# Performance work log

Measured on AMD Instinct MI355X. Metric: run time of the kernel, lower is better.

The kernel has to match this reference:

```python
import jax, jax.numpy as jnp
import numpy as np

N_NODES = 50000
N_EDGES = 800000
IN_DIM = 256
HID = 128
OUT = 128
LEAKY_SLOPE = 0.01


def setup_inputs() -> dict:
    key = jax.random.key(0)
    ks = jax.random.split(key, 12)
    s = 0.05
    return {
        "h": jax.random.normal(ks[0], (N_NODES, IN_DIM), dtype=jnp.float32),
        "src": jax.random.randint(ks[1], (N_EDGES,), 0, N_NODES, dtype=jnp.int32),
        "dst": jax.random.randint(ks[2], (N_EDGES,), 0, N_NODES, dtype=jnp.int32),
        "W1": jax.random.normal(ks[3], (HID, IN_DIM), dtype=jnp.float32) * s,
        "b1": jax.random.normal(ks[4], (HID,), dtype=jnp.float32) * s,
        "a1": jax.random.normal(ks[5], (2 * HID,), dtype=jnp.float32) * s,
        "ab1": jax.random.normal(ks[6], (), dtype=jnp.float32) * s,
        "W2": jax.random.normal(ks[7], (OUT, HID), dtype=jnp.float32) * s,
        "b2": jax.random.normal(ks[8], (OUT,), dtype=jnp.float32) * s,
        "a2": jax.random.normal(ks[9], (2 * OUT,), dtype=jnp.float32) * s,
        "ab2": jax.random.normal(ks[10], (), dtype=jnp.float32) * s,
    }


def gat_layer(h, src, dst, W, b, a, ab, n_nodes):
    # z = fc(h)
    z = h @ W.T + b                      # [N, D]
    D = z.shape[-1]
    zs = z[src]                           # [E, D] gather src features
    zd = z[dst]                           # [E, D] gather dst features
    # attn_fc(cat[zs, zd]) == zs @ a[:D] + zd @ a[D:] + ab
    e = zs @ a[:D] + zd @ a[D:] + ab      # [E]
    e = jnp.where(e > 0, e, LEAKY_SLOPE * e)  # leaky_relu, slope 0.01
    # segment softmax over edges grouped by destination node
    m = jax.ops.segment_max(e, dst, num_segments=n_nodes)   # [N]
    ex = jnp.exp(e - m[dst])                                  # [E]
    denom = jax.ops.segment_sum(ex, dst, num_segments=n_nodes)  # [N]
    alpha = ex / denom[dst]                                   # [E]
    # weighted scatter-sum of src features into dst nodes
    return jax.ops.segment_sum(alpha[:, None] * zs, dst, num_segments=n_nodes)


def reference(h, src, dst, W1, b1, a1, ab1, W2, b2, a2, ab2):
    n = h.shape[0]
    h1 = jax.nn.elu(gat_layer(h, src, dst, W1, b1, a1, ab1, n))
    h2 = jax.nn.elu(gat_layer(h1, src, dst, W2, b2, a2, ab2, n))
    return h2
```

## Files before the change

### kernel.cpp

```cpp
#include <hip/hip_runtime.h>
#include <hip/hip_bf16.h>

#define N_NODES 50000
#define N_EDGES 800000
#define IN_DIM  256
#define HID     128
#define LEAKY   0.01f

#define EDGE_BLOCKS  ((N_EDGES + 255) / 256)
#define NODE_WBLKS   (N_NODES / 4)
#define SCAN_BLOCKS  ((N_NODES + 255) / 256)
#define W1_ELEMS  (HID * IN_DIM)
#define W2_ELEMS  (HID * HID)

#define TM        96
#define FC_BLOCKS ((N_NODES + TM - 1) / TM)
#define LDA       72

typedef __attribute__((ext_vector_type(8))) short short8;
typedef __attribute__((ext_vector_type(4))) float f32x4;

__device__ __forceinline__ unsigned short f2bf(float x) {
    union { __hip_bfloat16 b; unsigned short u; } c;
    c.b = __float2bfloat16(x);
    return c.u;
}
__device__ __forceinline__ float bf2f(unsigned short u) {
    union { unsigned int u; float f; } c;
    c.u = ((unsigned int)u) << 16;
    return c.f;
}
__device__ __forceinline__ float2 bfu2(unsigned int u) {
    float2 r;
    r.x = bf2f((unsigned short)(u & 0xffff));
    r.y = bf2f((unsigned short)(u >> 16));
    return r;
}
__device__ __forceinline__ float lky(float x) { return x > 0.f ? x : LEAKY * x; }


__global__ void hist_split(const int* __restrict__ dst, int* __restrict__ counts,
                           int* __restrict__ erank,
                           const float* __restrict__ W1, unsigned short* __restrict__ w1hi,
                           unsigned short* __restrict__ w1lo,
                           const float* __restrict__ W2, unsigned short* __restrict__ w2hi,
                           unsigned short* __restrict__ w2lo) {
    int i = blockIdx.x * 256 + threadIdx.x;
    if (i < N_EDGES) erank[i] = atomicAdd(&counts[dst[i]], 1);
    if (i < W1_ELEMS) {
        float x = W1[i];
        unsigned short h = f2bf(x);
        w1hi[i] = h;
        w1lo[i] = f2bf(x - bf2f(h));
    } else if (i < W1_ELEMS + W2_ELEMS) {
        int j = i - W1_ELEMS;
        float x = W2[j];
        unsigned short h = f2bf(x);
        w2hi[j] = h;
        w2lo[j] = f2bf(x - bf2f(h));
    }
}

__global__ void scan_block(const int* __restrict__ counts, int* __restrict__ offsets,
                           int* __restrict__ bsums) {
    __shared__ int sh[256];
    int tid = threadIdx.x;
    int i = blockIdx.x * 256 + tid;
    int v = (i < N_NODES) ? counts[i] : 0;
    sh[tid] = v;
    __syncthreads();
    for (int o = 1; o < 256; o <<= 1) {
        int t = (tid >= o) ? sh[tid - o] : 0;
        __syncthreads();
        sh[tid] += t;
        __syncthreads();
    }
    if (i < N_NODES) offsets[i] = sh[tid] - v;
    if (tid == 255) bsums[blockIdx.x] = sh[255];
}

__global__ void scan_add(int* __restrict__ offsets, const int* __restrict__ bsums) {
    __shared__ int sh[256];
    int tid = threadIdx.x;
    int b = blockIdx.x;
    sh[tid] = (tid < b) ? bsums[tid] : 0;
    __syncthreads();
    for (int o = 128; o > 0; o >>= 1) {
        if (tid < o) sh[tid] += sh[tid + o];
        __syncthreads();
    }
    int base = sh[0];
    int i = b * 256 + tid;
    if (i < N_NODES) offsets[i] += base;
    if (i == N_NODES) offsets[N_NODES] = N_EDGES;
}

__global__ void fill_kernel(const int* __restrict__ dst, const int* __restrict__ src,
                            const int* __restrict__ erank,
                            const int* __restrict__ offsets,
                            int* __restrict__ csr_src) {
    int i = blockIdx.x * 256 + threadIdx.x;
    if (i < N_EDGES) {
        int d = dst[i];
        int slot = offsets[d] + erank[i];
        __builtin_nontemporal_store(src[i], &csr_src[slot]);
    }
}


__device__ __forceinline__ void epi(const f32x4* accn, int mbase, int q, int lane,
                                    const float* __restrict__ bias,
                                    const float* __restrict__ attn,
                                    unsigned short* __restrict__ Zb,
                                    float* __restrict__ sS, float* __restrict__ sD) {
    int r = lane & 15;
    int rowbase = mbase + (lane >> 4) * 4;
    float ps[4] = {0.f, 0.f, 0.f, 0.f};
    float pd[4] = {0.f, 0.f, 0.f, 0.f};
#pragma unroll
    for (int nt = 0; nt < 4; nt++) {
        int n = q * 64 + nt * 16 + r;
        float bn = bias[n];
        float aS = attn[n];
        float aD = attn[HID + n];
#pragma unroll
        for (int reg = 0; reg < 4; reg++) {
            float zv = accn[nt][reg] + bn;
            if (rowbase + reg < N_NODES)
                Zb[(size_t)(rowbase + reg) * HID + n] = f2bf(zv);
            ps[reg] += zv * aS;
            pd[reg] += zv * aD;
        }
    }
#pragma unroll
    for (int o = 1; o < 16; o <<= 1) {
#pragma unroll
        for (int reg = 0; reg < 4; reg++) {
            ps[reg] += __shfl_xor(ps[reg], o, 64);
            pd[reg] += __shfl_xor(pd[reg], o, 64);
        }
    }
    if (r == 0) {
#pragma unroll
        for (int reg = 0; reg < 4; reg++) {
            if (rowbase + reg < N_NODES) {
                sS[q * N_NODES + rowbase + reg] = ps[reg];
                sD[q * N_NODES + rowbase + reg] = pd[reg];
            }
        }
    }
}


__launch_bounds__(256)
__global__ void gemm_fc1(const float* __restrict__ A,
                         const unsigned short* __restrict__ Whi,
                         const unsigned short* __restrict__ Wlo,
                         const float* __restrict__ bias,
                         const float* __restrict__ attn,
                         unsigned short* __restrict__ Zb,
                         float* __restrict__ sS, float* __restrict__ sD) {
    __shared__ unsigned short Ah[TM * LDA];
    __shared__ unsigned short Al[TM * LDA];
    __shared__ unsigned short Bh[HID * LDA];
    __shared__ unsigned short Bl[HID * LDA];

    int tid  = threadIdx.x;
    int lane = tid & 63;
    int w    = tid >> 6;
    int q    = w & 1;
    int mh   = w >> 1;
    int m0   = blockIdx.x * TM;
    int r    = lane & 15;
    int koff = (lane >> 4) * 8;

    f32x4 acc[3][4];
#pragma unroll
    for (int s = 0; s < 3; s++)
#pragma unroll
        for (int nt = 0; nt < 4; nt++) acc[s][nt] = (f32x4){0.f, 0.f, 0.f, 0.f};

    for (int kc = 0; kc < IN_DIM / 64; kc++) {
        int k0 = kc * 64;
        __syncthreads();
#pragma unroll
        for (int j = 0; j < 6; j++) {
            int flat = j * 256 + tid;
            int row = flat >> 4;
            int c4 = (flat & 15) << 2;
            int gr = m0 + row;
            if (gr >= N_NODES) gr = N_NODES - 1;
            float4 v = *(const float4*)(A + (size_t)gr * IN_DIM + k0 + c4);
            unsigned short h0 = f2bf(v.x), h1 = f2bf(v.y), h2 = f2bf(v.z), h3 = f2bf(v.w);
            short4 hv = {(short)h0, (short)h1, (short)h2, (short)h3};
            short4 lv = {(short)f2bf(v.x - bf2f(h0)), (short)f2bf(v.y - bf2f(h1)),
                         (short)f2bf(v.z - bf2f(h2)), (short)f2bf(v.w - bf2f(h3))};
            *(short4*)&Ah[row * LDA + c4] = hv;
            *(short4*)&Al[row * LDA + c4] = lv;
        }
#pragma unroll
        for (int j = 0; j < 4; j++) {
            int flat = j * 256 + tid;
            int n = flat >> 3;
            int c8 = (flat & 7) << 3;
            *(short8*)&Bh[n * LDA + c8] = *(const short8*)(Whi + (size_t)n * IN_DIM + k0 + c8);
            *(short8*)&Bl[n * LDA + c8] = *(const short8*)(Wlo + (size_t)n * IN_DIM + k0 + c8);
        }
        __syncthreads();
#pragma unroll
        for (int ks = 0; ks < 2; ks++) {
            int kk = ks * 32 + koff;
            short8 ah[3], al[3], bh[4], bl[4];
#pragma unroll
            for (int s = 0; s < 3; s++) {
                int row = mh * 48 + s * 16 + r;
                ah[s] = *(const short8*)&Ah[row * LDA + kk];
                al[s] = *(const short8*)&Al[row * LDA + kk];
            }
#pragma unroll
            for (int nt = 0; nt < 4; nt++) {
                int n = q * 64 + nt * 16 + r;
                bh[nt] = *(const short8*)&Bh[n * LDA + kk];
                bl[nt] = *(const short8*)&Bl[n * LDA + kk];
            }
#pragma unroll
            for (int s = 0; s < 3; s++)
#pragma unroll
                for (int nt = 0; nt < 4; nt++) {
                    acc[s][nt] = __builtin_amdgcn_mfma_f32_16x16x32_bf16(ah[s], bh[nt], acc[s][nt], 0, 0, 0);
                    acc[s][nt] = __builtin_amdgcn_mfma_f32_16x16x32_bf16(al[s], bh[nt], acc[s][nt], 0, 0, 0);
                    acc[s][nt] = __builtin_amdgcn_mfma_f32_16x16x32_bf16(ah[s], bl[nt], acc[s][nt], 0, 0, 0);
                }
        }
    }
#pragma unroll
    for (int s = 0; s < 3; s++)
        epi(acc[s], m0 + mh * 48 + s * 16, q, lane, bias, attn, Zb, sS, sD);
}


__launch_bounds__(256)
__global__ void gemm_fc2(const unsigned short* __restrict__ Abf,
                         const unsigned short* __restrict__ Whi,
                         const unsigned short* __restrict__ Wlo,
                         const float* __restrict__ bias,
                         const float* __restrict__ attn,
                         unsigned short* __restrict__ Zb,
                         float* __restrict__ sS, float* __restrict__ sD) {
    __shared__ unsigned short Ah[TM * LDA];
    __shared__ unsigned short Bh[HID * LDA];
    __shared__ unsigned short Bl[HID * LDA];

    int tid  = threadIdx.x;
    int lane = tid & 63;
    int w    = tid >> 6;
    int q    = w & 1;
    int mh   = w >> 1;
    int m0   = blockIdx.x * TM;
    int r    = lane & 15;
    int koff = (lane >> 4) * 8;

    f32x4 acc[3][4];
#pragma unroll
    for (int s = 0; s < 3; s++)
#pragma unroll
        for (int nt = 0; nt < 4; nt++) acc[s][nt] = (f32x4){0.f, 0.f, 0.f, 0.f};

    for (int kc = 0; kc < HID / 64; kc++) {
        int k0 = kc * 64;
        __syncthreads();
#pragma unroll
        for (int j = 0; j < 3; j++) {
            int flat = j * 256 + tid;
            int row = flat >> 3;
            int c8 = (flat & 7) << 3;
            int gr = m0 + row;
            if (gr >= N_NODES) gr = N_NODES - 1;
            *(short8*)&Ah[row * LDA + c8] = *(const short8*)(Abf + (size_t)gr * HID + k0 + c8);
        }
#pragma unroll
        for (int j = 0; j < 4; j++) {
            int flat = j * 256 + tid;
            int n = flat >> 3;
            int c8 = (flat & 7) << 3;
            *(short8*)&Bh[n * LDA + c8] = *(const short8*)(Whi + (size_t)n * HID + k0 + c8);
            *(short8*)&Bl[n * LDA + c8] = *(const short8*)(Wlo + (size_t)n * HID + k0 + c8);
        }
        __syncthreads();
#pragma unroll
        for (int ks = 0; ks < 2; ks++) {
            int kk = ks * 32 + koff;
            short8 ah[3], bh[4], bl[4];
#pragma unroll
            for (int s = 0; s < 3; s++) {
                int row = mh * 48 + s * 16 + r;
                ah[s] = *(const short8*)&Ah[row * LDA + kk];
            }
#pragma unroll
            for (int nt = 0; nt < 4; nt++) {
                int n = q * 64 + nt * 16 + r;
                bh[nt] = *(const short8*)&Bh[n * LDA + kk];
                bl[nt] = *(const short8*)&Bl[n * LDA + kk];
            }
#pragma unroll
            for (int s = 0; s < 3; s++)
#pragma unroll
                for (int nt = 0; nt < 4; nt++) {
                    acc[s][nt] = __builtin_amdgcn_mfma_f32_16x16x32_bf16(ah[s], bh[nt], acc[s][nt], 0, 0, 0);
                    acc[s][nt] = __builtin_amdgcn_mfma_f32_16x16x32_bf16(ah[s], bl[nt], acc[s][nt], 0, 0, 0);
                }
        }
    }
#pragma unroll
    for (int s = 0; s < 3; s++)
        epi(acc[s], m0 + mh * 48 + s * 16, q, lane, bias, attn, Zb, sS, sD);
}


template <int OUT_BF>
__launch_bounds__(256)
__global__ void aggregate(const unsigned short* __restrict__ Zb,
                          const int* __restrict__ csr_src,
                          const int* __restrict__ offsets,
                          const float* __restrict__ sS,
                          const float* __restrict__ sD,
                          const float* __restrict__ ab,
                          unsigned short* __restrict__ OutBf,
                          float* __restrict__ OutF) {
    int v = blockIdx.x * 4 + (threadIdx.x >> 6);
    int lane = threadIdx.x & 63;
    int off = offsets[v];
    int deg = offsets[v + 1] - off;
    float sdv = sD[v] + sD[v + N_NODES] + ab[0];

    const unsigned int* Zrow = (const unsigned int*)Zb;
    float2 acc = {0.f, 0.f};

    if (deg <= 64) {
        bool act = lane < deg;
        int s_l = 0;
        float x = -3.0e38f;
        if (act) {
            s_l = csr_src[off + lane];
            x = lky(sS[s_l] + sS[s_l + N_NODES] + sdv);
        }
        float mx = x;
#pragma unroll
        for (int o = 32; o > 0; o >>= 1) mx = fmaxf(mx, __shfl_xor(mx, o, 64));
        float ex = act ? __expf(x - mx) : 0.f;
        float sum = ex;
#pragma unroll
        for (int o = 32; o > 0; o >>= 1) sum += __shfl_xor(sum, o, 64);
        float al_l = (deg > 0) ? ex / sum : 0.f;

        int t = 0;
        for (; t + 8 <= deg; t += 8) {
            int   s[8];
            float a[8];
            unsigned int rw[8];
#pragma unroll
            for (int j = 0; j < 8; j++) {
                s[j] = __shfl(s_l, t + j, 64);
                a[j] = __shfl(al_l, t + j, 64);
            }
#pragma unroll
            for (int j = 0; j < 8; j++)
                rw[j] = Zrow[(size_t)s[j] * (HID / 2) + lane];
#pragma unroll
            for (int j = 0; j < 8; j++) {
                float2 zz = bfu2(rw[j]);
                acc.x += a[j] * zz.x;
                acc.y += a[j] * zz.y;
            }
        }
        for (; t < deg; t++) {
            int sj = __shfl(s_l, t, 64);
            float aj = __shfl(al_l, t, 64);
            float2 zz = bfu2(Zrow[(size_t)sj * (HID / 2) + lane]);
            acc.x += aj * zz.x;
            acc.y += aj * zz.y;
        }
    } else {
        float mx = -3.0e38f;
        for (int t = lane; t < deg; t += 64) {
            int s = csr_src[off + t];
            mx = fmaxf(mx, lky(sS[s] + sS[s + N_NODES] + sdv));
        }
#pragma unroll
        for (int o = 32; o > 0; o >>= 1) mx = fmaxf(mx, __shfl_xor(mx, o, 64));
        float sum = 0.f;
        for (int t = lane; t < deg; t += 64) {
            int s = csr_src[off + t];
            sum += __expf(lky(sS[s] + sS[s + N_NODES] + sdv) - mx);
        }
#pragma unroll
        for (int o = 32; o > 0; o >>= 1) sum += __shfl_xor(sum, o, 64);
        float inv = 1.f / sum;
        for (int t = 0; t < deg; t++) {
            int s = csr_src[off + t];
            float al = __expf(lky(sS[s] + sS[s + N_NODES] + sdv) - mx) * inv;
            float2 zz = bfu2(Zrow[(size_t)s * (HID / 2) + lane]);
            acc.x += al * zz.x;
            acc.y += al * zz.y;
        }
    }

    acc.x = acc.x > 0.f ? acc.x : __expf(acc.x) - 1.f;
    acc.y = acc.y > 0.f ? acc.y : __expf(acc.y) - 1.f;

    if (OUT_BF) {
        ushort2 o2;
        o2.x = f2bf(acc.x);
        o2.y = f2bf(acc.y);
        *((ushort2*)(OutBf + (size_t)v * HID + lane * 2)) = o2;
    } else {
        float2 o2 = {acc.x, acc.y};
        *((float2*)(OutF + (size_t)v * HID + lane * 2)) = o2;
    }
}


extern "C" void kernel_launch(void* const* d_in, const int* in_sizes, int n_in,
                              void* d_out, int out_size, void* d_ws, size_t ws_size,
                              hipStream_t stream) {
    const float* h   = (const float*)d_in[0];
    const int*   src = (const int*)d_in[1];
    const int*   dst = (const int*)d_in[2];
    const float* W1  = (const float*)d_in[3];
    const float* b1  = (const float*)d_in[4];
    const float* a1  = (const float*)d_in[5];
    const float* ab1 = (const float*)d_in[6];
    const float* W2  = (const float*)d_in[7];
    const float* b2  = (const float*)d_in[8];
    const float* a2  = (const float*)d_in[9];
    const float* ab2 = (const float*)d_in[10];
    float* out = (float*)d_out;

    unsigned short* zb = (unsigned short*)d_ws;
    float* sS = (float*)(zb + (size_t)N_NODES * HID);
    float* sD = sS + 2 * N_NODES;
    int* counts  = (int*)(sD + 2 * N_NODES);
    int* offsets = counts + N_NODES;
    int* bsums   = offsets + N_NODES + 16;
    unsigned short* h1   = (unsigned short*)(bsums + 256);
    unsigned short* w1hi = h1 + (size_t)N_NODES * HID;
    unsigned short* w1lo = w1hi + W1_ELEMS;
    unsigned short* w2hi = w1lo + W1_ELEMS;
    unsigned short* w2lo = w2hi + W2_ELEMS;
    int* csr_src = (int*)(w2lo + W2_ELEMS);
    int* erank   = csr_src + N_EDGES;

    hipMemsetAsync(counts, 0, (size_t)N_NODES * sizeof(int), stream);

    hist_split<<<EDGE_BLOCKS, 256, 0, stream>>>(dst, counts, erank,
                                                W1, w1hi, w1lo, W2, w2hi, w2lo);
    scan_block<<<SCAN_BLOCKS, 256, 0, stream>>>(counts, offsets, bsums);
    scan_add<<<SCAN_BLOCKS, 256, 0, stream>>>(offsets, bsums);
    fill_kernel<<<EDGE_BLOCKS, 256, 0, stream>>>(dst, src, erank, offsets, csr_src);

    gemm_fc1<<<FC_BLOCKS, 256, 0, stream>>>(h, w1hi, w1lo, b1, a1, zb, sS, sD);
    aggregate<1><<<NODE_WBLKS, 256, 0, stream>>>(zb, csr_src, offsets, sS, sD, ab1, h1, nullptr);

    gemm_fc2<<<FC_BLOCKS, 256, 0, stream>>>(h1, w2hi, w2lo, b2, a2, zb, sS, sD);
    aggregate<0><<<NODE_WBLKS, 256, 0, stream>>>(zb, csr_src, offsets, sS, sD, ab2, nullptr, out);
}
```

Measured before the change: 290.2 us.

## Combine per-half attention scores in shared memory and widen aggregate gather unroll

```diff
diff --git a/kernel.cpp b/kernel.cpp
--- a/kernel.cpp
+++ b/kernel.cpp
@@ -37,6 +37,9 @@
     return r;
 }
 __device__ __forceinline__ float lky(float x) { return x > 0.f ? x : LEAKY * x; }
+__device__ __forceinline__ float rl_f(float v, int l) {
+    return __int_as_float(__builtin_amdgcn_readlane(__float_as_int(v), l));
+}
 
 
 __global__ void hist_split(const int* __restrict__ dst, int* __restrict__ counts,
@@ -108,13 +111,13 @@
 }
 
 
-__device__ __forceinline__ void epi(const f32x4* accn, int mbase, int q, int lane,
+__device__ __forceinline__ void epi(const f32x4* accn, int lrow0, int m0, int q, int lane,
                                     const float* __restrict__ bias,
                                     const float* __restrict__ attn,
                                     unsigned short* __restrict__ Zb,
-                                    float* __restrict__ sS, float* __restrict__ sD) {
+                                    float* __restrict__ sbuf) {
     int r = lane & 15;
-    int rowbase = mbase + (lane >> 4) * 4;
+    int lrowbase = lrow0 + (lane >> 4) * 4;
     float ps[4] = {0.f, 0.f, 0.f, 0.f};
     float pd[4] = {0.f, 0.f, 0.f, 0.f};
 #pragma unroll
@@ -126,8 +129,8 @@
 #pragma unroll
         for (int reg = 0; reg < 4; reg++) {
             float zv = accn[nt][reg] + bn;
-            if (rowbase + reg < N_NODES)
-                Zb[(size_t)(rowbase + reg) * HID + n] = f2bf(zv);
+            if (m0 + lrowbase + reg < N_NODES)
+                Zb[(size_t)(m0 + lrowbase + reg) * HID + n] = f2bf(zv);
             ps[reg] += zv * aS;
             pd[reg] += zv * aD;
         }
@@ -143,10 +146,19 @@
     if (r == 0) {
 #pragma unroll
         for (int reg = 0; reg < 4; reg++) {
-            if (rowbase + reg < N_NODES) {
-                sS[q * N_NODES + rowbase + reg] = ps[reg];
-                sD[q * N_NODES + rowbase + reg] = pd[reg];
-            }
+            sbuf[q * 192 + lrowbase + reg] = ps[reg];
+            sbuf[q * 192 + 96 + lrowbase + reg] = pd[reg];
+        }
+    }
+}
+
+__device__ __forceinline__ void score_combine(const float* __restrict__ sbuf, int tid, int m0,
+                                              float* __restrict__ sS, float* __restrict__ sD) {
+    if (tid < 96) {
+        int gr = m0 + tid;
+        if (gr < N_NODES) {
+            sS[gr] = sbuf[tid] + sbuf[192 + tid];
+            sD[gr] = sbuf[96 + tid] + sbuf[192 + 96 + tid];
         }
     }
 }
@@ -233,9 +245,13 @@
                 }
         }
     }
+    __syncthreads();
+    float* sbuf = (float*)Ah;
 #pragma unroll
     for (int s = 0; s < 3; s++)
-        epi(acc[s], m0 + mh * 48 + s * 16, q, lane, bias, attn, Zb, sS, sD);
+        epi(acc[s], mh * 48 + s * 16, m0, q, lane, bias, attn, Zb, sbuf);
+    __syncthreads();
+    score_combine(sbuf, tid, m0, sS, sD);
 }
 
 
@@ -311,9 +327,13 @@
                 }
         }
     }
+    __syncthreads();
+    float* sbuf = (float*)Ah;
 #pragma unroll
     for (int s = 0; s < 3; s++)
-        epi(acc[s], m0 + mh * 48 + s * 16, q, lane, bias, attn, Zb, sS, sD);
+        epi(acc[s], mh * 48 + s * 16, m0, q, lane, bias, attn, Zb, sbuf);
+    __syncthreads();
+    score_combine(sbuf, tid, m0, sS, sD);
 }
 
 
@@ -331,7 +351,7 @@
     int lane = threadIdx.x & 63;
     int off = offsets[v];
     int deg = offsets[v + 1] - off;
-    float sdv = sD[v] + sD[v + N_NODES] + ab[0];
+    float sdv = sD[v] + ab[0];
 
     const unsigned int* Zrow = (const unsigned int*)Zb;
     float2 acc = {0.f, 0.f};
@@ -342,7 +362,7 @@
         float x = -3.0e38f;
         if (act) {
             s_l = csr_src[off + lane];
-            x = lky(sS[s_l] + sS[s_l + N_NODES] + sdv);
+            x = lky(sS[s_l] + sdv);
         }
         float mx = x;
 #pragma unroll
@@ -354,28 +374,47 @@
         float al_l = (deg > 0) ? ex / sum : 0.f;
 
         int t = 0;
-        for (; t + 8 <= deg; t += 8) {
-            int   s[8];
-            float a[8];
-            unsigned int rw[8];
-#pragma unroll
-            for (int j = 0; j < 8; j++) {
-                s[j] = __shfl(s_l, t + j, 64);
-                a[j] = __shfl(al_l, t + j, 64);
-            }
-#pragma unroll
-            for (int j = 0; j < 8; j++)
+        for (; t + 16 <= deg; t += 16) {
+            int   s[16];
+            float a[16];
+            unsigned int rw[16];
+#pragma unroll
+            for (int j = 0; j < 16; j++) {
+                s[j] = __builtin_amdgcn_readlane(s_l, t + j);
+                a[j] = rl_f(al_l, t + j);
+            }
+#pragma unroll
+            for (int j = 0; j < 16; j++)
                 rw[j] = Zrow[(size_t)s[j] * (HID / 2) + lane];
 #pragma unroll
-            for (int j = 0; j < 8; j++) {
+            for (int j = 0; j < 16; j++) {
                 float2 zz = bfu2(rw[j]);
                 acc.x += a[j] * zz.x;
                 acc.y += a[j] * zz.y;
             }
         }
+        for (; t + 4 <= deg; t += 4) {
+            int   s[4];
+            float a[4];
+            unsigned int rw[4];
+#pragma unroll
+            for (int j = 0; j < 4; j++) {
+                s[j] = __builtin_amdgcn_readlane(s_l, t + j);
+                a[j] = rl_f(al_l, t + j);
+            }
+#pragma unroll
+            for (int j = 0; j < 4; j++)
+                rw[j] = Zrow[(size_t)s[j] * (HID / 2) + lane];
+#pragma unroll
+            for (int j = 0; j < 4; j++) {
+                float2 zz = bfu2(rw[j]);
+                acc.x += a[j] * zz.x;
+                acc.y += a[j] * zz.y;
+            }
+        }
         for (; t < deg; t++) {
-            int sj = __shfl(s_l, t, 64);
-            float aj = __shfl(al_l, t, 64);
+            int sj = __builtin_amdgcn_readlane(s_l, t);
+            float aj = rl_f(al_l, t);
             float2 zz = bfu2(Zrow[(size_t)sj * (HID / 2) + lane]);
             acc.x += aj * zz.x;
             acc.y += aj * zz.y;
@@ -384,21 +423,21 @@
         float mx = -3.0e38f;
         for (int t = lane; t < deg; t += 64) {
             int s = csr_src[off + t];
-            mx = fmaxf(mx, lky(sS[s] + sS[s + N_NODES] + sdv));
+            mx = fmaxf(mx, lky(sS[s] + sdv));
         }
 #pragma unroll
         for (int o = 32; o > 0; o >>= 1) mx = fmaxf(mx, __shfl_xor(mx, o, 64));
         float sum = 0.f;
         for (int t = lane; t < deg; t += 64) {
             int s = csr_src[off + t];
-            sum += __expf(lky(sS[s] + sS[s + N_NODES] + sdv) - mx);
+            sum += __expf(lky(sS[s] + sdv) - mx);
         }
 #pragma unroll
         for (int o = 32; o > 0; o >>= 1) sum += __shfl_xor(sum, o, 64);
         float inv = 1.f / sum;
         for (int t = 0; t < deg; t++) {
             int s = csr_src[off + t];
-            float al = __expf(lky(sS[s] + sS[s + N_NODES] + sdv) - mx) * inv;
+            float al = __expf(lky(sS[s] + sdv) - mx) * inv;
             float2 zz = bfu2(Zrow[(size_t)s * (HID / 2) + lane]);
             acc.x += al * zz.x;
             acc.y += al * zz.y;
@@ -438,8 +477,8 @@
 
     unsigned short* zb = (unsigned short*)d_ws;
     float* sS = (float*)(zb + (size_t)N_NODES * HID);
-    float* sD = sS + 2 * N_NODES;
-    int* counts  = (int*)(sD + 2 * N_NODES);
+    float* sD = sS + N_NODES;
+    int* counts  = (int*)(sD + N_NODES);
     int* offsets = counts + N_NODES;
     int* bsums   = offsets + N_NODES + 16;
     unsigned short* h1   = (unsigned short*)(bsums + 256);
```

After: 282.3 us. -2.7%, faster.
